# Optimization experiments

Measured on AMD Instinct MI355X. Metric: run time of the kernel, lower is better.

The kernel has to match this reference:

```python
import jax, jax.numpy as jnp
import numpy as np

B, S, D_IN, D_OUT, HID, E, SHARE, TOPK = 4, 2048, 1024, 1024, 2048, 8, 1, 2


def setup_inputs() -> dict:
    key = jax.random.key(0)
    ks = jax.random.split(key, 12)
    s_in = 1.0 / np.sqrt(D_IN)
    s_hid = 1.0 / np.sqrt(HID)
    return {
        "x": jax.random.normal(ks[0], (B, S, D_IN), jnp.float32),
        "gate_w": jax.random.normal(ks[1], (D_IN, E), jnp.float32) * s_in,
        "gate_b": jnp.zeros((E,), jnp.float32),
        "ew1": jax.random.normal(ks[2], (E, D_IN, HID), jnp.float32) * s_in,
        "eb1": jnp.zeros((E, HID), jnp.float32),
        "ew2": jax.random.normal(ks[3], (E, HID, D_OUT), jnp.float32) * s_hid,
        "eb2": jnp.zeros((E, D_OUT), jnp.float32),
        "sw1": jax.random.normal(ks[4], (SHARE, D_IN, HID), jnp.float32) * s_in,
        "sb1": jnp.zeros((SHARE, HID), jnp.float32),
        "sw2": jax.random.normal(ks[5], (SHARE, HID, D_OUT), jnp.float32) * s_hid,
        "sb2": jnp.zeros((SHARE, D_OUT), jnp.float32),
        "top_k": TOPK,
    }


def reference(x, gate_w, gate_b, ew1, eb1, ew2, eb2, sw1, sb1, sw2, sb2, top_k):
    Bx, Sx, Din = x.shape
    flat_x = x.reshape(-1, Din)                      # [T, D]
    T = flat_x.shape[0]
    Ex = gate_w.shape[1]

    # gate + softmax + top-k, renormalize top-k weights
    logits = flat_x @ gate_w + gate_b                # [T, E]
    expert_weights = jax.nn.softmax(logits, axis=-1)
    topv, topi = jax.lax.top_k(expert_weights, top_k)
    topv = topv / jnp.sum(topv, axis=-1, keepdims=True)

    # per-token combine weights scattered into [T, E] (zero for unselected)
    combine = jnp.zeros((T, Ex), flat_x.dtype)
    combine = combine.at[jnp.arange(T)[:, None], topi].add(topv)

    # expert MLPs (BasicExpert: Linear -> ReLU -> Linear), batched over experts
    h = jax.nn.relu(jnp.einsum("td,edh->teh", flat_x, ew1) + eb1)   # [T, E, H]
    eo = jnp.einsum("teh,eho->teo", h, ew2) + eb2                    # [T, E, O]
    moe_out = jnp.einsum("teo,te->to", eo, combine)                  # [T, O]
    final = moe_out.reshape(Bx, Sx, -1)

    # shared experts added densely to every token
    for k in range(sw1.shape[0]):
        sh = jax.nn.relu(jnp.einsum("bsd,dh->bsh", x, sw1[k]) + sb1[k])
        final = final + jnp.einsum("bsh,ho->bso", sh, sw2[k]) + sb2[k]

    return final, expert_weights
```

## Files before the change

kernel.cpp:

```cpp
#include <hip/hip_runtime.h>
#include <hip/hip_bf16.h>
#include <stdint.h>

#define T_TOK 8192
#define DIN   1024
#define DOUT  1024
#define HID   2048
#define NEXP  8
#define MAXN  8192

typedef __attribute__((ext_vector_type(8))) short short8;
typedef __attribute__((ext_vector_type(4))) float floatx4;

__device__ __forceinline__ ushort f2bf(float f) {
    uint32_t u = __float_as_uint(f);
    uint32_t r = (u + 0x7fffu + ((u >> 16) & 1u)) >> 16;
    return (ushort)r;
}

__device__ __forceinline__ void load_lds_16(const ushort* g, ushort* l) {
    __builtin_amdgcn_global_load_lds(
        (const __attribute__((address_space(1))) void*)g,
        (__attribute__((address_space(3))) void*)l, 16, 0, 0);
}

__global__ void convert_x_kernel(const float* __restrict__ in, ushort* __restrict__ out, int n4) {
    int i = blockIdx.x * blockDim.x + threadIdx.x;
    if (i >= n4) return;
    float4 v = ((const float4*)in)[i];
    ushort4 o;
    o.x = f2bf(v.x); o.y = f2bf(v.y); o.z = f2bf(v.z); o.w = f2bf(v.w);
    ((ushort4*)out)[i] = o;
}

__global__ void transpose_bf16_kernel(const float* __restrict__ in, ushort* __restrict__ out,
                                      int R, int C) {
    __shared__ float tile[64][65];
    size_t base = (size_t)blockIdx.z * R * C;
    in  += base;
    out += base;
    int r0 = blockIdx.y * 64, c0 = blockIdx.x * 64;
    int t  = threadIdx.x;
    int rr = t >> 4;
    int cc = (t & 15) * 4;
    for (int p = 0; p < 4; p++) {
        int row = rr + p * 16;
        float4 v = *(const float4*)(in + (size_t)(r0 + row) * C + c0 + cc);
        tile[row][cc + 0] = v.x; tile[row][cc + 1] = v.y;
        tile[row][cc + 2] = v.z; tile[row][cc + 3] = v.w;
    }
    __syncthreads();
    for (int p = 0; p < 4; p++) {
        int orow = rr + p * 16;
        ushort4 o;
        o.x = f2bf(tile[cc + 0][orow]);
        o.y = f2bf(tile[cc + 1][orow]);
        o.z = f2bf(tile[cc + 2][orow]);
        o.w = f2bf(tile[cc + 3][orow]);
        *(ushort4*)(out + (size_t)(c0 + orow) * R + r0 + cc) = o;
    }
}

__global__ void gate_compute_kernel(const float* __restrict__ x, const float* __restrict__ gw,
                                    const float* __restrict__ gb, float* __restrict__ ew_out,
                                    int* __restrict__ te1, int* __restrict__ te2,
                                    float* __restrict__ tw1, float* __restrict__ tw2) {
    int gid  = blockIdx.x * blockDim.x + threadIdx.x;
    int t    = gid >> 6;
    int lane = threadIdx.x & 63;
    if (t >= T_TOK) return;
    float acc[8];
    #pragma unroll
    for (int e = 0; e < 8; e++) acc[e] = 0.f;
    const float* xrow = x + (size_t)t * DIN;
    #pragma unroll
    for (int i = 0; i < 16; i++) {
        int d = lane + i * 64;
        float xv = xrow[d];
        const float4* wr = (const float4*)(gw + (size_t)d * 8);
        float4 w0 = wr[0], w1 = wr[1];
        acc[0] += xv * w0.x; acc[1] += xv * w0.y; acc[2] += xv * w0.z; acc[3] += xv * w0.w;
        acc[4] += xv * w1.x; acc[5] += xv * w1.y; acc[6] += xv * w1.z; acc[7] += xv * w1.w;
    }
    #pragma unroll
    for (int e = 0; e < 8; e++)
        #pragma unroll
        for (int off = 32; off; off >>= 1) acc[e] += __shfl_xor(acc[e], off);
    if (lane == 0) {
        float l[8], mx = -1e30f;
        #pragma unroll
        for (int e = 0; e < 8; e++) { l[e] = acc[e] + gb[e]; mx = fmaxf(mx, l[e]); }
        float s = 0.f;
        #pragma unroll
        for (int e = 0; e < 8; e++) { l[e] = expf(l[e] - mx); s += l[e]; }
        float inv = 1.f / s;
        #pragma unroll
        for (int e = 0; e < 8; e++) { l[e] *= inv; ew_out[(size_t)t * 8 + e] = l[e]; }
        int i1 = 0;
        #pragma unroll
        for (int e = 1; e < 8; e++) if (l[e] > l[i1]) i1 = e;
        int i2 = (i1 == 0) ? 1 : 0;
        #pragma unroll
        for (int e = 0; e < 8; e++) if (e != i1 && l[e] > l[i2]) i2 = e;
        float s2 = l[i1] + l[i2];
        te1[t] = i1; tw1[t] = l[i1] / s2;
        te2[t] = i2; tw2[t] = l[i2] / s2;
    }
}

__global__ void build_lists_kernel(const int* __restrict__ te1, const int* __restrict__ te2,
                                   const float* __restrict__ tw1, const float* __restrict__ tw2,
                                   int* __restrict__ counts, int* __restrict__ etok,
                                   float* __restrict__ ew) {
    __shared__ int lcnt[NEXP];
    __shared__ int gbase[NEXP];
    int tid = threadIdx.x;
    int t = blockIdx.x * 256 + tid;
    if (tid < NEXP) lcnt[tid] = 0;
    __syncthreads();
    int e1 = te1[t], e2 = te2[t];
    float w1 = tw1[t], w2 = tw2[t];
    int r1 = atomicAdd(&lcnt[e1], 1);
    int r2 = atomicAdd(&lcnt[e2], 1);
    __syncthreads();
    if (tid < NEXP) gbase[tid] = atomicAdd(&counts[tid], lcnt[tid]);
    __syncthreads();
    int s1 = gbase[e1] + r1;
    etok[e1 * MAXN + s1] = t;
    ew  [e1 * MAXN + s1] = w1;
    int s2 = gbase[e2] + r2;
    etok[e2 * MAXN + s2] = t;
    ew  [e2 * MAXN + s2] = w2;
}

__global__ void prefix_kernel(const int* __restrict__ counts, int* __restrict__ offsets) {
    if (threadIdx.x == 0 && blockIdx.x == 0) {
        int o = 0;
        for (int e = 0; e < NEXP; e++) { offsets[e] = o; o += counts[e]; }
    }
}

template <int MODE>
__global__ __launch_bounds__(256)
void gemm_kernel(const ushort* __restrict__ A, const ushort* __restrict__ Bt,
                 const float* __restrict__ bias, ushort* __restrict__ Hout,
                 float* __restrict__ Out,
                 const int* __restrict__ counts, const int* __restrict__ offsets,
                 const int* __restrict__ expert_tok, const float* __restrict__ expert_w,
                 int K) {
    const int e = blockIdx.z;
    int cnt, rowbase = 0;
    size_t bt_off = 0;
    const float* bcol = bias;
    if constexpr (MODE == 0) {
        cnt = counts[e]; rowbase = offsets[e];
        bt_off = (size_t)e * HID * DIN; bcol = bias + (size_t)e * HID;
    } else if constexpr (MODE == 1) {
        cnt = T_TOK;
    } else if constexpr (MODE == 2) {
        cnt = counts[e]; rowbase = offsets[e];
        bt_off = (size_t)e * DOUT * HID; bcol = bias + (size_t)e * DOUT;
    } else {
        cnt = T_TOK;
    }

    const int m0 = blockIdx.y * 128;
    if (m0 >= cnt) return;
    const int n0 = blockIdx.x * 128;

    __shared__ ushort As[8192];
    __shared__ ushort Bs[8192];
    __shared__ int    rowA[128];
    __shared__ int    rowTok[128];
    __shared__ float  rowW[128];

    const int tid = threadIdx.x;
    if (tid < 128) {
        int g = m0 + tid;
        if constexpr (MODE == 0) {
            rowA[tid] = (g < cnt) ? expert_tok[e * MAXN + g] : 0;
        } else if constexpr (MODE == 1) {
            rowA[tid] = g;
        } else if constexpr (MODE == 2) {
            rowA[tid]   = (g < cnt) ? (rowbase + g) : rowbase;
            rowTok[tid] = (g < cnt) ? expert_tok[e * MAXN + g] : 0;
            rowW[tid]   = (g < cnt) ? expert_w[e * MAXN + g] : 0.f;
        } else {
            rowA[tid] = g;
        }
    }
    __syncthreads();

    const int wave = tid >> 6, lane = tid & 63;
    const int lm = lane & 15, lq = lane >> 4;

    const ushort* gA[4];
    const ushort* gB[4];
    ushort* dA[4];
    ushort* dB[4];
    #pragma unroll
    for (int i = 0; i < 4; i++) {
        int b = wave * 4 + i;
        int rblk = b >> 1, kkb = b & 1;
        int r = rblk * 16 + lm;
        gA[i] = A + (size_t)rowA[r] * K + kkb * 32 + lq * 8;
        gB[i] = Bt + bt_off + (size_t)(n0 + r) * K + kkb * 32 + lq * 8;
        dA[i] = &As[b * 512];
        dB[i] = &Bs[b * 512];
    }

    floatx4 acc[4][4];
    #pragma unroll
    for (int i = 0; i < 4; i++)
        #pragma unroll
        for (int j = 0; j < 4; j++) acc[i][j] = (floatx4){0.f, 0.f, 0.f, 0.f};

    for (int k0 = 0; k0 < K; k0 += 64) {
        #pragma unroll
        for (int i = 0; i < 4; i++) {
            load_lds_16(gA[i] + k0, dA[i]);
            load_lds_16(gB[i] + k0, dB[i]);
        }
        __syncthreads();
        #pragma unroll
        for (int kkb = 0; kkb < 2; kkb++) {
            short8 afr[4], bfr[4];
            #pragma unroll
            for (int mt = 0; mt < 4; mt++)
                afr[mt] = *(const short8*)&As[(((wave >> 1) * 4 + mt) * 2 + kkb) * 512 + lane * 8];
            #pragma unroll
            for (int nt = 0; nt < 4; nt++)
                bfr[nt] = *(const short8*)&Bs[(((wave & 1) * 4 + nt) * 2 + kkb) * 512 + lane * 8];
            #pragma unroll
            for (int mt = 0; mt < 4; mt++)
                #pragma unroll
                for (int nt = 0; nt < 4; nt++)
                    acc[mt][nt] = __builtin_amdgcn_mfma_f32_16x16x32_bf16(
                        afr[mt], bfr[nt], acc[mt][nt], 0, 0, 0);
        }
        __syncthreads();
    }

    const int wm = (wave >> 1) * 64, wn = (wave & 1) * 64;
    #pragma unroll
    for (int mt = 0; mt < 4; mt++) {
        int rl_base = wm + mt * 16 + lq * 4;
        #pragma unroll
        for (int nt = 0; nt < 4; nt++) {
            int col = n0 + wn + nt * 16 + lm;
            float bv = bcol[col];
            #pragma unroll
            for (int r = 0; r < 4; r++) {
                int rl = rl_base + r;
                int g  = m0 + rl;
                float v = acc[mt][nt][r];
                if constexpr (MODE == 0) {
                    if (g < cnt) {
                        v = fmaxf(v + bv, 0.f);
                        Hout[(size_t)(rowbase + g) * HID + col] = f2bf(v);
                    }
                } else if constexpr (MODE == 1) {
                    v = fmaxf(v + bv, 0.f);
                    Hout[(size_t)g * HID + col] = f2bf(v);
                } else if constexpr (MODE == 2) {
                    if (g < cnt) {
                        v = (v + bv) * rowW[rl];
                        atomicAdd(&Out[(size_t)rowTok[rl] * DOUT + col], v);
                    }
                } else {
                    atomicAdd(&Out[(size_t)g * DOUT + col], v + bv);
                }
            }
        }
    }
}

extern "C" void kernel_launch(void* const* d_in, const int* in_sizes, int n_in,
                              void* d_out, int out_size, void* d_ws, size_t ws_size,
                              hipStream_t stream) {
    const float* x   = (const float*)d_in[0];
    const float* gw  = (const float*)d_in[1];
    const float* gb  = (const float*)d_in[2];
    const float* ew1 = (const float*)d_in[3];
    const float* eb1 = (const float*)d_in[4];
    const float* ew2 = (const float*)d_in[5];
    const float* eb2 = (const float*)d_in[6];
    const float* sw1 = (const float*)d_in[7];
    const float* sb1 = (const float*)d_in[8];
    const float* sw2 = (const float*)d_in[9];
    const float* sb2 = (const float*)d_in[10];

    float* out_final = (float*)d_out;
    float* out_ew    = out_final + (size_t)T_TOK * DOUT;

    char* ws = (char*)d_ws;
    size_t off = 0;
    auto alloc = [&](size_t bytes) -> void* {
        void* p = ws + off;
        off += (bytes + 255) & ~(size_t)255;
        return p;
    };
    ushort* x_bf    = (ushort*)alloc((size_t)T_TOK * DIN * 2);
    ushort* ew1t    = (ushort*)alloc((size_t)NEXP * HID * DIN * 2);
    ushort* ew2t    = (ushort*)alloc((size_t)NEXP * DOUT * HID * 2);
    ushort* sw1t    = (ushort*)alloc((size_t)HID * DIN * 2);
    ushort* sw2t    = (ushort*)alloc((size_t)DOUT * HID * 2);
    ushort* h_buf   = (ushort*)alloc((size_t)T_TOK * 2 * HID * 2);
    ushort* sh_buf  = (ushort*)alloc((size_t)T_TOK * HID * 2);
    int*    counts  = (int*)alloc(NEXP * 4);
    int*    offsets = (int*)alloc(NEXP * 4);
    int*    etok    = (int*)alloc((size_t)NEXP * MAXN * 4);
    float*  ew      = (float*)alloc((size_t)NEXP * MAXN * 4);
    int*    te1     = (int*)alloc((size_t)T_TOK * 4);
    int*    te2     = (int*)alloc((size_t)T_TOK * 4);
    float*  tw1     = (float*)alloc((size_t)T_TOK * 4);
    float*  tw2     = (float*)alloc((size_t)T_TOK * 4);

    hipMemsetAsync(d_out, 0, (size_t)T_TOK * DOUT * 4, stream);
    hipMemsetAsync(counts, 0, NEXP * 4, stream);

    convert_x_kernel<<<(T_TOK * DIN / 4) / 256, 256, 0, stream>>>(x, x_bf, T_TOK * DIN / 4);
    transpose_bf16_kernel<<<dim3(HID / 64, DIN / 64, NEXP), 256, 0, stream>>>(ew1, ew1t, DIN, HID);
    transpose_bf16_kernel<<<dim3(DOUT / 64, HID / 64, NEXP), 256, 0, stream>>>(ew2, ew2t, HID, DOUT);
    transpose_bf16_kernel<<<dim3(HID / 64, DIN / 64, 1), 256, 0, stream>>>(sw1, sw1t, DIN, HID);
    transpose_bf16_kernel<<<dim3(DOUT / 64, HID / 64, 1), 256, 0, stream>>>(sw2, sw2t, HID, DOUT);

    gate_compute_kernel<<<T_TOK / 4, 256, 0, stream>>>(x, gw, gb, out_ew, te1, te2, tw1, tw2);
    build_lists_kernel<<<T_TOK / 256, 256, 0, stream>>>(te1, te2, tw1, tw2, counts, etok, ew);
    prefix_kernel<<<1, 64, 0, stream>>>(counts, offsets);

    gemm_kernel<0><<<dim3(HID / 128, MAXN / 128, NEXP), 256, 0, stream>>>(
        x_bf, ew1t, eb1, h_buf, nullptr, counts, offsets, etok, ew, DIN);
    gemm_kernel<1><<<dim3(HID / 128, T_TOK / 128, 1), 256, 0, stream>>>(
        x_bf, sw1t, sb1, sh_buf, nullptr, counts, offsets, etok, ew, DIN);
    gemm_kernel<2><<<dim3(DOUT / 128, MAXN / 128, NEXP), 256, 0, stream>>>(
        h_buf, ew2t, eb2, nullptr, out_final, counts, offsets, etok, ew, HID);
    gemm_kernel<3><<<dim3(DOUT / 128, T_TOK / 128, 1), 256, 0, stream>>>(
        sh_buf, sw2t, sb2, nullptr, out_final, counts, offsets, etok, ew, HID);
}
```

Measured before the change: 800.0 us.

## Merge routed and shared expert GEMMs into one launch per layer

Combines the routed-expert and shared-expert GEMMs for each layer into a single launch using a flat 1D grid. Expert index is interleaved into the low bits of the block id so active expert tiles spread across CUs, and shared-expert tiles are appended after them. Hidden activations go into one shared buffer, and per-row token and weight lookups move from LDS into the epilogue. The aim is fewer launches and better load balance, at the cost of many early-exit blocks and extra global reads in the epilogue.

```diff
diff --git a/kernel.cpp b/kernel.cpp
--- a/kernel.cpp
+++ b/kernel.cpp
@@ -140,54 +140,57 @@
     }
 }
 
-template <int MODE>
+template <int LAYER>
 __global__ __launch_bounds__(256)
-void gemm_kernel(const ushort* __restrict__ A, const ushort* __restrict__ Bt,
-                 const float* __restrict__ bias, ushort* __restrict__ Hout,
-                 float* __restrict__ Out,
+void gemm_kernel(const ushort* __restrict__ A, const ushort* __restrict__ BtE,
+                 const ushort* __restrict__ BtS,
+                 const float* __restrict__ biasE, const float* __restrict__ biasS,
+                 ushort* __restrict__ Hout, float* __restrict__ Out,
                  const int* __restrict__ counts, const int* __restrict__ offsets,
-                 const int* __restrict__ expert_tok, const float* __restrict__ expert_w,
-                 int K) {
-    const int e = blockIdx.z;
-    int cnt, rowbase = 0;
-    size_t bt_off = 0;
-    const float* bcol = bias;
-    if constexpr (MODE == 0) {
-        cnt = counts[e]; rowbase = offsets[e];
-        bt_off = (size_t)e * HID * DIN; bcol = bias + (size_t)e * HID;
-    } else if constexpr (MODE == 1) {
+                 const int* __restrict__ etok, const float* __restrict__ eww) {
+    constexpr int K    = (LAYER == 1) ? DIN : HID;
+    constexpr int N    = (LAYER == 1) ? HID : DOUT;
+    constexpr int NB_N = N / 128;
+    constexpr int RB   = NEXP * (MAXN / 128) * NB_N;
+
+    const int bid = (int)blockIdx.x;
+    const bool routed = bid < RB;
+    int e = 0, m0, n0, cnt, rowbase = 0;
+    const ushort* Bt;
+    const float* bcol;
+    if (routed) {
+        e = bid & 7;
+        int r = bid >> 3;
+        m0 = (r / NB_N) * 128;
+        n0 = (r % NB_N) * 128;
+        cnt = counts[e];
+        if (m0 >= cnt) return;
+        rowbase = offsets[e];
+        Bt = BtE + (size_t)e * N * K;
+        bcol = biasE + (size_t)e * N;
+    } else {
+        int r = bid - RB;
+        m0 = (r / NB_N) * 128;
+        n0 = (r % NB_N) * 128;
         cnt = T_TOK;
-    } else if constexpr (MODE == 2) {
-        cnt = counts[e]; rowbase = offsets[e];
-        bt_off = (size_t)e * DOUT * HID; bcol = bias + (size_t)e * DOUT;
-    } else {
-        cnt = T_TOK;
-    }
-
-    const int m0 = blockIdx.y * 128;
-    if (m0 >= cnt) return;
-    const int n0 = blockIdx.x * 128;
+        Bt = BtS;
+        bcol = biasS;
+    }
 
     __shared__ ushort As[8192];
     __shared__ ushort Bs[8192];
     __shared__ int    rowA[128];
-    __shared__ int    rowTok[128];
-    __shared__ float  rowW[128];
 
     const int tid = threadIdx.x;
     if (tid < 128) {
         int g = m0 + tid;
-        if constexpr (MODE == 0) {
-            rowA[tid] = (g < cnt) ? expert_tok[e * MAXN + g] : 0;
-        } else if constexpr (MODE == 1) {
-            rowA[tid] = g;
-        } else if constexpr (MODE == 2) {
-            rowA[tid]   = (g < cnt) ? (rowbase + g) : rowbase;
-            rowTok[tid] = (g < cnt) ? expert_tok[e * MAXN + g] : 0;
-            rowW[tid]   = (g < cnt) ? expert_w[e * MAXN + g] : 0.f;
+        int row;
+        if constexpr (LAYER == 1) {
+            row = routed ? ((g < cnt) ? etok[e * MAXN + g] : 0) : g;
         } else {
-            rowA[tid] = g;
+            row = routed ? (rowbase + ((g < cnt) ? g : 0)) : (T_TOK * 2 + g);
         }
+        rowA[tid] = row;
     }
     __syncthreads();
 
@@ -204,7 +207,7 @@
         int rblk = b >> 1, kkb = b & 1;
         int r = rblk * 16 + lm;
         gA[i] = A + (size_t)rowA[r] * K + kkb * 32 + lq * 8;
-        gB[i] = Bt + bt_off + (size_t)(n0 + r) * K + kkb * 32 + lq * 8;
+        gB[i] = Bt + (size_t)(n0 + r) * K + kkb * 32 + lq * 8;
         dA[i] = &As[b * 512];
         dB[i] = &Bs[b * 512];
     }
@@ -254,21 +257,22 @@
                 int rl = rl_base + r;
                 int g  = m0 + rl;
                 float v = acc[mt][nt][r];
-                if constexpr (MODE == 0) {
-                    if (g < cnt) {
+                if constexpr (LAYER == 1) {
+                    if (!routed || g < cnt) {
                         v = fmaxf(v + bv, 0.f);
-                        Hout[(size_t)(rowbase + g) * HID + col] = f2bf(v);
-                    }
-                } else if constexpr (MODE == 1) {
-                    v = fmaxf(v + bv, 0.f);
-                    Hout[(size_t)g * HID + col] = f2bf(v);
-                } else if constexpr (MODE == 2) {
-                    if (g < cnt) {
-                        v = (v + bv) * rowW[rl];
-                        atomicAdd(&Out[(size_t)rowTok[rl] * DOUT + col], v);
+                        int orow = routed ? (rowbase + g) : (T_TOK * 2 + g);
+                        Hout[(size_t)orow * HID + col] = f2bf(v);
                     }
                 } else {
-                    atomicAdd(&Out[(size_t)g * DOUT + col], v + bv);
+                    if (routed) {
+                        if (g < cnt) {
+                            int   tok = etok[e * MAXN + g];
+                            float w   = eww[e * MAXN + g];
+                            atomicAdd(&Out[(size_t)tok * DOUT + col], (v + bv) * w);
+                        }
+                    } else {
+                        atomicAdd(&Out[(size_t)g * DOUT + col], v + bv);
+                    }
                 }
             }
         }
@@ -305,12 +309,11 @@
     ushort* ew2t    = (ushort*)alloc((size_t)NEXP * DOUT * HID * 2);
     ushort* sw1t    = (ushort*)alloc((size_t)HID * DIN * 2);
     ushort* sw2t    = (ushort*)alloc((size_t)DOUT * HID * 2);
-    ushort* h_buf   = (ushort*)alloc((size_t)T_TOK * 2 * HID * 2);
-    ushort* sh_buf  = (ushort*)alloc((size_t)T_TOK * HID * 2);
+    ushort* h_all   = (ushort*)alloc((size_t)T_TOK * 3 * HID * 2);
     int*    counts  = (int*)alloc(NEXP * 4);
     int*    offsets = (int*)alloc(NEXP * 4);
     int*    etok    = (int*)alloc((size_t)NEXP * MAXN * 4);
-    float*  ew      = (float*)alloc((size_t)NEXP * MAXN * 4);
+    float*  eww     = (float*)alloc((size_t)NEXP * MAXN * 4);
     int*    te1     = (int*)alloc((size_t)T_TOK * 4);
     int*    te2     = (int*)alloc((size_t)T_TOK * 4);
     float*  tw1     = (float*)alloc((size_t)T_TOK * 4);
@@ -326,15 +329,11 @@
     transpose_bf16_kernel<<<dim3(DOUT / 64, HID / 64, 1), 256, 0, stream>>>(sw2, sw2t, HID, DOUT);
 
     gate_compute_kernel<<<T_TOK / 4, 256, 0, stream>>>(x, gw, gb, out_ew, te1, te2, tw1, tw2);
-    build_lists_kernel<<<T_TOK / 256, 256, 0, stream>>>(te1, te2, tw1, tw2, counts, etok, ew);
+    build_lists_kernel<<<T_TOK / 256, 256, 0, stream>>>(te1, te2, tw1, tw2, counts, etok, eww);
     prefix_kernel<<<1, 64, 0, stream>>>(counts, offsets);
 
-    gemm_kernel<0><<<dim3(HID / 128, MAXN / 128, NEXP), 256, 0, stream>>>(
-        x_bf, ew1t, eb1, h_buf, nullptr, counts, offsets, etok, ew, DIN);
-    gemm_kernel<1><<<dim3(HID / 128, T_TOK / 128, 1), 256, 0, stream>>>(
-        x_bf, sw1t, sb1, sh_buf, nullptr, counts, offsets, etok, ew, DIN);
-    gemm_kernel<2><<<dim3(DOUT / 128, MAXN / 128, NEXP), 256, 0, stream>>>(
-        h_buf, ew2t, eb2, nullptr, out_final, counts, offsets, etok, ew, HID);
-    gemm_kernel<3><<<dim3(DOUT / 128, T_TOK / 128, 1), 256, 0, stream>>>(
-        sh_buf, sw2t, sb2, nullptr, out_final, counts, offsets, etok, ew, HID);
-}
+    gemm_kernel<1><<<NEXP * 64 * 16 + 64 * 16, 256, 0, stream>>>(
+        x_bf, ew1t, sw1t, eb1, sb1, h_all, nullptr, counts, offsets, etok, eww);
+    gemm_kernel<2><<<NEXP * 64 * 8 + 64 * 8, 256, 0, stream>>>(
+        h_all, ew2t, sw2t, eb2, sb2, nullptr, out_final, counts, offsets, etok, eww);
+}
```

Measured after the change: 851.8 us. 1.06x slower.
